# Optimization experiments

Hardware: AMD Instinct MI355X
Metric: run time of the kernel (lower is better)

The kernel has to match this reference:

```python
import jax, jax.numpy as jnp
import numpy as np

N, E, G, IN, H, L, C = 20000, 320000, 128, 16, 64, 4, 10
AVG_D_LOG = float(np.log(17.0))  # log(avg_degree + 1)


def setup_inputs() -> dict:
    key = jax.random.key(0)
    ks = jax.random.split(key, 24)
    p = lambda k, shape: jax.random.normal(k, shape, dtype=jnp.float32) * 0.05
    return dict(
        h=jax.random.normal(ks[0], (N, IN), jnp.float32),
        snorm_n=jax.random.uniform(ks[1], (N, 1), jnp.float32, 0.05, 1.0),
        embW=p(ks[2], (IN, H)), embB=p(ks[3], (H,)),
        preW=p(ks[4], (L, 2 * H, H)), preB=p(ks[5], (L, H)),
        postW=p(ks[6], (L, 13 * H, H)), postB=p(ks[7], (L, H)),
        mixW=p(ks[8], (L, H, H)), mixB=p(ks[9], (L, H)),
        r1W=p(ks[10], (H, H // 2)), r1B=p(ks[11], (H // 2,)),
        r2W=p(ks[12], (H // 2, H // 4)), r2B=p(ks[13], (H // 4,)),
        r3W=p(ks[14], (H // 4, C)), r3B=p(ks[15], (C,)),
        src=jax.random.randint(ks[16], (E,), 0, N),
        dst=jax.random.randint(ks[17], (E,), 0, N),
        graph_ids=jnp.sort(jax.random.randint(ks[18], (N,), 0, G)),
    )


def _pna_forward(h, snorm_n, embW, embB, preW, preB, postW, postB, mixW, mixB,
                 r1W, r1B, r2W, r2B, r3W, r3B, src, dst, graph_ids):
    # Degree-based scalers (computed once; graph is fixed across layers)
    deg = jax.ops.segment_sum(jnp.ones((E,), h.dtype), dst, num_segments=N)  # [N]
    degc = jnp.maximum(deg, 1.0)[:, None]
    logd = jnp.log(deg + 1.0)
    amp = (logd / AVG_D_LOG)[:, None]                      # amplification scaler
    att = (AVG_D_LOG / jnp.maximum(logd, 1e-5))[:, None]   # attenuation scaler
    has_nb = (deg > 0.0)[:, None]

    x = h @ embW + embB  # node embedding [N, H]
    for i in range(L):
        x_in = x
        # pretrans: per-edge message from cat(h_src, h_dst)  [E, H]
        m = jnp.concatenate([x[src], x[dst]], axis=-1) @ preW[i] + preB[i]
        # multi-aggregator reduce at dst: mean, max, min, std
        mean = jax.ops.segment_sum(m, dst, num_segments=N) / degc
        msq = jax.ops.segment_sum(m * m, dst, num_segments=N) / degc
        std = jnp.sqrt(jax.nn.relu(msq - mean * mean) + 1e-5)
        mx = jnp.where(has_nb, jax.ops.segment_max(m, dst, num_segments=N), 0.0)
        mn = jnp.where(has_nb, jax.ops.segment_min(m, dst, num_segments=N), 0.0)
        agg = jnp.concatenate([mean, mx, mn, std], axis=-1)  # [N, 4H]
        # degree scalers: identity, amplification, attenuation -> [N, 12H]
        scaled = jnp.concatenate([agg, agg * amp, agg * att], axis=-1)
        # posttrans over cat(scaled_agg, h) -> [N, H]
        y = jnp.concatenate([scaled, x], axis=-1) @ postW[i] + postB[i]
        # tower mixing network (LeakyReLU FC)
        y = jax.nn.leaky_relu(y @ mixW[i] + mixB[i])
        y = y * snorm_n          # graph norm
        x = x_in + y             # residual
    # mean-nodes readout per graph
    gsum = jax.ops.segment_sum(x, graph_ids, num_segments=G)
    cnt = jnp.maximum(jax.ops.segment_sum(jnp.ones((N,), x.dtype), graph_ids, num_segments=G), 1.0)
    hg = gsum / cnt[:, None]
    # MLPReadout: two halving ReLU layers + classifier
    hg = jax.nn.relu(hg @ r1W + r1B)
    hg = jax.nn.relu(hg @ r2W + r2B)
    return hg @ r3W + r3B  # [G, C]


def reference(h, snorm_n, embW, embB, preW, preB, postW, postB, mixW, mixB,
              r1W, r1B, r2W, r2B, r3W, r3B, src, dst, graph_ids):
    return _pna_forward(h, snorm_n, embW, embB, preW, preB, postW, postB,
                        mixW, mixB, r1W, r1B, r2W, r2B, r3W, r3B,
                        src, dst, graph_ids)
```

## Files before the change

kernel.cpp:

```cpp
#include <hip/hip_runtime.h>
#include <math.h>

#define N_ 20000
#define E_ 320000
#define G_ 128
#define IN_ 16
#define H_ 64
#define L_ 4
#define C_ 10
#define AVG_D_LOG 2.8332133440562162f

union F4 { float4 v; float f[4]; };

typedef _Float16 h8 __attribute__((ext_vector_type(8)));
typedef _Float16 h4 __attribute__((ext_vector_type(4)));
typedef float f4x __attribute__((ext_vector_type(4)));
#define MFMA16(a, b, c) __builtin_amdgcn_mfma_f32_16x16x32_f16((a), (b), (c), 0, 0, 0)


__global__ __launch_bounds__(256) void k_setup(
    const float* __restrict__ h, const float* __restrict__ embW, const float* __restrict__ embB,
    float* __restrict__ x,
    const float* __restrict__ preW, const float* __restrict__ postW, const float* __restrict__ mixW,
    _Float16* __restrict__ preWT, _Float16* __restrict__ postWT, _Float16* __restrict__ mixWT,
    int* __restrict__ zbase) {
  int bb = blockIdx.x, tid = threadIdx.x;
  if (bb < 5000) {
    int n = bb * 4 + (tid >> 6);
    int c = tid & 63;
    float acc = embB[c];
#pragma unroll
    for (int k = 0; k < IN_; k++) acc += h[n * IN_ + k] * embW[k * H_ + c];
    x[n * H_ + c] = acc;
  } else if (bb < 6024) {
    int idx = (bb - 5000) * 256 + tid;
    if (idx < 32768) {
      int l = idx >> 13, r = idx & 8191;
      int c = r >> 6, k = r & 63;
      preWT[idx] = (_Float16)preW[l * 8192 + k * 64 + c];
    } else if (idx < 245760) {
      int j = idx - 32768;
      int l = j / 53248, r = j % 53248;
      int c = r / 832, k = r % 832;
      postWT[j] = (_Float16)postW[l * 53248 + k * 64 + c];
    } else {
      int j = idx - 245760;
      int l = j >> 12, r = j & 4095;
      int c = r >> 6, k = r & 63;
      mixWT[j] = (_Float16)mixW[l * 4096 + k * 64 + c];
    }
  } else {
    int i = (bb - 6024) * 256 + tid;
    if (i < 2 * N_) zbase[i] = 0;
  }
}


__global__ __launch_bounds__(256) void k_hist(const int* __restrict__ dst, int* __restrict__ deg) {
  int e = blockIdx.x * 256 + threadIdx.x;
  if (e < E_) atomicAdd(&deg[dst[e]], 1);
}


__global__ __launch_bounds__(1024) void k_scan(const int* __restrict__ deg, int* __restrict__ offs) {
  __shared__ int sh[1024];
  int t = threadIdx.x;
  int base = t * 20;
  int local[20];
  int s = 0;
  if (t < 1000) {
#pragma unroll
    for (int c = 0; c < 5; c++) {
      int4 v = *(const int4*)(deg + base + c * 4);
      local[c * 4 + 0] = s; s += v.x;
      local[c * 4 + 1] = s; s += v.y;
      local[c * 4 + 2] = s; s += v.z;
      local[c * 4 + 3] = s; s += v.w;
    }
  }
  sh[t] = s;
  __syncthreads();
  for (int off = 1; off < 1024; off <<= 1) {
    int v = (t >= off) ? sh[t - off] : 0;
    __syncthreads();
    sh[t] += v;
    __syncthreads();
  }
  if (t < 1000) {
    int excl = sh[t] - s;
#pragma unroll
    for (int c = 0; c < 5; c++) {
      int4 o;
      o.x = excl + local[c * 4 + 0];
      o.y = excl + local[c * 4 + 1];
      o.z = excl + local[c * 4 + 2];
      o.w = excl + local[c * 4 + 3];
      *(int4*)(offs + base + c * 4) = o;
    }
  }
  if (t == 0) offs[N_] = sh[1023];
}


__global__ __launch_bounds__(256) void k_mix(
    const int* __restrict__ src, const int* __restrict__ dst,
    const int* __restrict__ offs, int* __restrict__ cursor, int* __restrict__ csr,
    const int* __restrict__ deg,
    float* __restrict__ ampv, float* __restrict__ attv,
    float* __restrict__ invd, float* __restrict__ hnb,
    const float* __restrict__ x, const _Float16* __restrict__ preWT,
    const float* __restrict__ preB, _Float16* __restrict__ ah, float* __restrict__ b) {
  int bb = blockIdx.x, tid = threadIdx.x;
  if (bb < 1250) {
    int e = bb * 256 + tid;
    if (e < E_) {
      int d = dst[e];
      int pos = offs[d] + atomicAdd(&cursor[d], 1);
      csr[pos] = src[e];
    }
  } else if (bb < 1329) {
    int idx = (bb - 1250) * 256 + tid;
    if (idx < N_) {
      float d = (float)deg[idx];
      float logd = logf(d + 1.f);
      ampv[idx] = logd / AVG_D_LOG;
      attv[idx] = AVG_D_LOG / fmaxf(logd, 1e-5f);
      invd[idx] = 1.f / fmaxf(d, 1.f);
      hnb[idx] = d > 0.f ? 1.f : 0.f;
    }
  } else {
    int n0 = (bb - 1329) * 32;
    int lane = tid & 63, wv = tid >> 6;
    int mt = wv & 1, nh = wv >> 1;
    int l15 = lane & 15, k0q = (lane >> 4) * 8;
    int mrow = n0 + mt * 16 + l15;
    const float* xr = x + (size_t)mrow * 64;
    const _Float16* wb0 = preWT + (size_t)(nh * 64 + l15) * 64 + k0q;
    f4x acc0 = {0.f,0.f,0.f,0.f}, acc1 = {0.f,0.f,0.f,0.f}, acc2 = {0.f,0.f,0.f,0.f}, acc3 = {0.f,0.f,0.f,0.f};
#pragma unroll
    for (int kb = 0; kb < 64; kb += 32) {
      int ko = kb + k0q;
      F4 xa, xb2;
      xa.v = *(const float4*)(xr + ko);
      xb2.v = *(const float4*)(xr + ko + 4);
      h8 af;
      af[0]=(_Float16)xa.f[0]; af[1]=(_Float16)xa.f[1]; af[2]=(_Float16)xa.f[2]; af[3]=(_Float16)xa.f[3];
      af[4]=(_Float16)xb2.f[0]; af[5]=(_Float16)xb2.f[1]; af[6]=(_Float16)xb2.f[2]; af[7]=(_Float16)xb2.f[3];
      acc0 = MFMA16(af, *(const h8*)(wb0 + kb), acc0);
      acc1 = MFMA16(af, *(const h8*)(wb0 + 1024 + kb), acc1);
      acc2 = MFMA16(af, *(const h8*)(wb0 + 2048 + kb), acc2);
      acc3 = MFMA16(af, *(const h8*)(wb0 + 3072 + kb), acc3);
    }
    int rbase = n0 + mt * 16 + (lane >> 4) * 4;
    f4x accs[4] = {acc0, acc1, acc2, acc3};
#pragma unroll
    for (int t = 0; t < 4; t++) {
      int col = nh * 64 + t * 16 + l15;
#pragma unroll
      for (int r = 0; r < 4; r++) {
        int n = rbase + r;
        if (col < 64) ah[(size_t)n * 64 + col] = (_Float16)accs[t][r];
        else          b[(size_t)n * 64 + (col - 64)] = accs[t][r] + preB[col - 64];
      }
    }
  }
}


__global__ __launch_bounds__(256, 4) void k_layer(
    const _Float16* __restrict__ ahin, const float* __restrict__ bin,
    const int* __restrict__ offs, const int* __restrict__ csr,
    const float* __restrict__ invd, const float* __restrict__ hnb,
    const _Float16* __restrict__ WT, const float* __restrict__ Bv,
    const _Float16* __restrict__ mixWT, const float* __restrict__ mixB,
    const float* __restrict__ ampv, const float* __restrict__ attv,
    const float* __restrict__ snorm, float* __restrict__ x,
    const _Float16* __restrict__ preWT, const float* __restrict__ preB,
    _Float16* __restrict__ ahout, float* __restrict__ bout, int do_pre) {
  __shared__ _Float16 aggs[16 * 280];
  __shared__ _Float16 ys[16 * 88];
  __shared__ _Float16 xs[16 * 88];
  __shared__ _Float16 xt[16 * 72];
  __shared__ int csr_s[1024];
  __shared__ int soffs[17];
  int tid = threadIdx.x;
  int n0 = blockIdx.x * 16;
  int lane = tid & 63, wv = tid >> 6;

  int e0 = offs[n0];
  int ecnt = offs[n0 + 16] - e0;
  {
    int row = tid >> 4, qq = tid & 15;
    F4 xv; xv.v = *(const float4*)(x + (size_t)(n0 + row) * 64 + qq * 4);
    h4 xh;
    xh[0] = (_Float16)xv.f[0]; xh[1] = (_Float16)xv.f[1];
    xh[2] = (_Float16)xv.f[2]; xh[3] = (_Float16)xv.f[3];
    *(h4*)(xt + row * 72 + qq * 4) = xh;
  }
  if (tid < 17) soffs[tid] = offs[n0 + tid];
  {
    int cnt = ecnt < 1024 ? ecnt : 1024;
    for (int i = tid; i < cnt; i += 256) csr_s[i] = csr[e0 + i];
  }
  __syncthreads();

  {
    int nl = tid >> 4, q = tid & 15;
    int n = n0 + nl;
    int o0 = soffs[nl];
    int deg = soffs[nl + 1] - o0;
    float inv = invd[n], hn = hnb[n];
    F4 bv; bv.v = *(const float4*)(bin + (size_t)n * 64 + q * 4);
    float sum[4], sq[4], mx[4], mn[4];
#pragma unroll
    for (int i = 0; i < 4; i++) {
      sum[i] = 0.f; sq[i] = 0.f;
      mx[i] = -__builtin_inff(); mn[i] = __builtin_inff();
    }
#define ACC4_(S0, S1, S2, S3)                                            \
    do {                                                                 \
      h4 a0 = *(const h4*)(ahin + (size_t)(S0) * 64 + q * 4);            \
      h4 a1 = *(const h4*)(ahin + (size_t)(S1) * 64 + q * 4);            \
      h4 a2 = *(const h4*)(ahin + (size_t)(S2) * 64 + q * 4);            \
      h4 a3 = *(const h4*)(ahin + (size_t)(S3) * 64 + q * 4);            \
      _Pragma("unroll")                                                  \
      for (int i = 0; i < 4; i++) {                                      \
        float v0 = (float)a0[i], v1 = (float)a1[i];                      \
        float v2 = (float)a2[i], v3 = (float)a3[i];                      \
        sum[i] += (v0 + v1) + (v2 + v3);                                 \
        sq[i] += v0 * v0; sq[i] += v1 * v1;                              \
        sq[i] += v2 * v2; sq[i] += v3 * v3;                              \
        mx[i] = fmaxf(mx[i], fmaxf(fmaxf(v0, v1), fmaxf(v2, v3)));       \
        mn[i] = fminf(mn[i], fminf(fminf(v0, v1), fminf(v2, v3)));       \
      }                                                                  \
    } while (0)
#define ACC1_(S0)                                                        \
    do {                                                                 \
      h4 a0 = *(const h4*)(ahin + (size_t)(S0) * 64 + q * 4);            \
      _Pragma("unroll")                                                  \
      for (int i = 0; i < 4; i++) {                                      \
        float v0 = (float)a0[i];                                         \
        sum[i] += v0; sq[i] += v0 * v0;                                  \
        mx[i] = fmaxf(mx[i], v0); mn[i] = fminf(mn[i], v0);              \
      }                                                                  \
    } while (0)
    if (ecnt <= 1024) {
      int lo = o0 - e0;
      int j = 0;
      for (; j + 3 < deg; j += 4) {
        int s0 = csr_s[lo + j], s1 = csr_s[lo + j + 1];
        int s2 = csr_s[lo + j + 2], s3 = csr_s[lo + j + 3];
        ACC4_(s0, s1, s2, s3);
      }
      for (; j < deg; j++) { int s0 = csr_s[lo + j]; ACC1_(s0); }
    } else {
      int j = 0;
      for (; j + 3 < deg; j += 4) {
        int s0 = csr[o0 + j], s1 = csr[o0 + j + 1];
        int s2 = csr[o0 + j + 2], s3 = csr[o0 + j + 3];
        ACC4_(s0, s1, s2, s3);
      }
      for (; j < deg; j++) { int s0 = csr[o0 + j]; ACC1_(s0); }
    }
#undef ACC4_
#undef ACC1_
    h4 hm, hx, hmn, hs;
#pragma unroll
    for (int i = 0; i < 4; i++) {
      float mean_a = sum[i] * inv;
      float var = sq[i] * inv - mean_a * mean_a;
      hs[i] = (_Float16)sqrtf(fmaxf(var, 0.f) + 1e-5f);
      bool nb = hn > 0.5f;
      hm[i] = (_Float16)(nb ? (mean_a + bv.f[i]) : 0.f);
      hx[i] = (_Float16)(nb ? (mx[i] + bv.f[i]) : 0.f);
      hmn[i] = (_Float16)(nb ? (mn[i] + bv.f[i]) : 0.f);
    }
    _Float16* ap = aggs + nl * 280 + q * 4;
    *(h4*)(ap) = hm;
    *(h4*)(ap + 64) = hx;
    *(h4*)(ap + 128) = hmn;
    *(h4*)(ap + 192) = hs;
  }
  __syncthreads();

  int nh = wv;
  int l15 = lane & 15, k0q = (lane >> 4) * 8;
  const _Float16* ag = aggs + (size_t)l15 * 280 + k0q;
  int col0 = nh * 16 + l15;
  const _Float16* w0 = WT + (size_t)col0 * 832 + k0q;
  f4x aI = {0.f,0.f,0.f,0.f}, aA = {0.f,0.f,0.f,0.f}, aT = {0.f,0.f,0.f,0.f};
#pragma unroll 4
  for (int kb = 0; kb < 256; kb += 32) {
    h8 af = *(const h8*)(ag + kb);
    aI = MFMA16(af, *(const h8*)(w0 + kb), aI);
    aA = MFMA16(af, *(const h8*)(w0 + 256 + kb), aA);
    aT = MFMA16(af, *(const h8*)(w0 + 512 + kb), aT);
  }
  const _Float16* xtr = xt + (size_t)l15 * 72 + k0q;
#pragma unroll
  for (int kb = 0; kb < 64; kb += 32) {
    h8 af = *(const h8*)(xtr + kb);
    aI = MFMA16(af, *(const h8*)(w0 + 768 + kb), aI);
  }
  int qr = (lane >> 4) * 4;
  int rbase = n0 + qr;
  int yrow = qr;
  float b0 = Bv[col0];
#pragma unroll
  for (int r = 0; r < 4; r++) {
    int n = rbase + r;
    float amp = ampv[n], att = attv[n];
    ys[(yrow + r) * 88 + col0] = (_Float16)(aI[r] + b0 + amp * aA[r] + att * aT[r]);
  }
  __syncthreads();
  f4x m0 = {0.f,0.f,0.f,0.f};
  const _Float16* yr = ys + (size_t)l15 * 88 + k0q;
  const _Float16* mw0 = mixWT + (size_t)col0 * 64 + k0q;
#pragma unroll
  for (int kb = 0; kb < 64; kb += 32) {
    h8 af = *(const h8*)(yr + kb);
    m0 = MFMA16(af, *(const h8*)(mw0 + kb), m0);
  }
  float mb0 = mixB[col0];
#pragma unroll
  for (int r = 0; r < 4; r++) {
    int n = rbase + r;
    float sn = snorm[n];
    float t0 = m0[r] + mb0; t0 = t0 > 0.f ? t0 : 0.01f * t0;
    float* xp = x + (size_t)n * 64;
    float xo0 = xp[col0] + t0 * sn;
    xp[col0] = xo0;
    xs[(yrow + r) * 88 + col0] = (_Float16)xo0;
  }

  if (do_pre) {
    __syncthreads();
    int ch = wv;
    const _Float16* xf = xs + (size_t)l15 * 88 + k0q;
    const _Float16* wb0 = preWT + (size_t)(ch * 32 + l15) * 64 + k0q;
    f4x p0 = {0.f,0.f,0.f,0.f}, p1 = {0.f,0.f,0.f,0.f};
#pragma unroll
    for (int kb = 0; kb < 64; kb += 32) {
      h8 af = *(const h8*)(xf + kb);
      p0 = MFMA16(af, *(const h8*)(wb0 + kb), p0);
      p1 = MFMA16(af, *(const h8*)(wb0 + 1024 + kb), p1);
    }
    int prb = n0 + (lane >> 4) * 4;
    f4x accs[2] = {p0, p1};
#pragma unroll
    for (int t = 0; t < 2; t++) {
      int col = ch * 32 + t * 16 + l15;
#pragma unroll
      for (int r = 0; r < 4; r++) {
        int n = prb + r;
        if (col < 64) ahout[(size_t)n * 64 + col] = (_Float16)accs[t][r];
        else          bout[(size_t)n * 64 + (col - 64)] = accs[t][r] + preB[col - 64];
      }
    }
  }
}


__device__ inline int lower_bound_gid(const int* __restrict__ gid, int val) {
  int lo = 0, hi = N_;
  while (lo < hi) {
    int mid = (lo + hi) >> 1;
    if (gid[mid] < val) lo = mid + 1; else hi = mid;
  }
  return lo;
}

__global__ __launch_bounds__(256) void k_readout_fused(
    const float* __restrict__ x, const int* __restrict__ gid,
    const float* __restrict__ r1W, const float* __restrict__ r1B,
    const float* __restrict__ r2W, const float* __restrict__ r2B,
    const float* __restrict__ r3W, const float* __restrict__ r3B,
    float* __restrict__ out) {
  __shared__ float part[4 * 64];
  __shared__ float hg[64];
  __shared__ float t1[32];
  __shared__ float t2[16];
  int g = blockIdx.x, tid = threadIdx.x;
  int lo = lower_bound_gid(gid, g);
  int hi = lower_bound_gid(gid, g + 1);
  int c = tid & 63, w = tid >> 6;
  float s = 0.f;
  for (int n = lo + w; n < hi; n += 4) s += x[(size_t)n * 64 + c];
  part[w * 64 + c] = s;
  __syncthreads();
  if (w == 0) {
    float tot = part[c] + part[64 + c] + part[128 + c] + part[192 + c];
    float cnt = (float)(hi - lo);
    if (cnt < 1.f) cnt = 1.f;
    hg[c] = tot / cnt;
  }
  __syncthreads();
  if (tid < 32) {
    float acc = r1B[tid];
#pragma unroll 8
    for (int k = 0; k < 64; k++) acc += hg[k] * r1W[k * 32 + tid];
    t1[tid] = fmaxf(acc, 0.f);
  }
  __syncthreads();
  if (tid < 16) {
    float acc = r2B[tid];
#pragma unroll 8
    for (int k = 0; k < 32; k++) acc += t1[k] * r2W[k * 16 + tid];
    t2[tid] = fmaxf(acc, 0.f);
  }
  __syncthreads();
  if (tid < 10) {
    float acc = r3B[tid];
#pragma unroll
    for (int k = 0; k < 16; k++) acc += t2[k] * r3W[k * 10 + tid];
    out[g * 10 + tid] = acc;
  }
}


extern "C" void kernel_launch(void* const* d_in, const int* in_sizes, int n_in,
                              void* d_out, int out_size, void* d_ws, size_t ws_size,
                              hipStream_t stream) {
  const float* h     = (const float*)d_in[0];
  const float* snorm = (const float*)d_in[1];
  const float* embW  = (const float*)d_in[2];
  const float* embB  = (const float*)d_in[3];
  const float* preW  = (const float*)d_in[4];
  const float* preB  = (const float*)d_in[5];
  const float* postW = (const float*)d_in[6];
  const float* postB = (const float*)d_in[7];
  const float* mixW  = (const float*)d_in[8];
  const float* mixB  = (const float*)d_in[9];
  const float* r1W   = (const float*)d_in[10];
  const float* r1B   = (const float*)d_in[11];
  const float* r2W   = (const float*)d_in[12];
  const float* r2B   = (const float*)d_in[13];
  const float* r3W   = (const float*)d_in[14];
  const float* r3B   = (const float*)d_in[15];
  const int* src     = (const int*)d_in[16];
  const int* dst     = (const int*)d_in[17];
  const int* gid     = (const int*)d_in[18];
  float* out = (float*)d_out;

  char* w = (char*)d_ws;
  float* x        = (float*)w; w += (size_t)N_ * 64 * 4;
  _Float16* ah0   = (_Float16*)w; w += (size_t)N_ * 64 * 2;
  _Float16* ah1   = (_Float16*)w; w += (size_t)N_ * 64 * 2;
  float* b0       = (float*)w; w += (size_t)N_ * 64 * 4;
  float* b1       = (float*)w; w += (size_t)N_ * 64 * 4;
  _Float16* preWT = (_Float16*)w; w += (size_t)4 * 128 * 64 * 2;
  _Float16* postWT= (_Float16*)w; w += (size_t)4 * 64 * 832 * 2;
  _Float16* mixWT = (_Float16*)w; w += (size_t)4 * 64 * 64 * 2;
  float* ampv = (float*)w; w += (size_t)N_ * 4;
  float* attv = (float*)w; w += (size_t)N_ * 4;
  float* invd = (float*)w; w += (size_t)N_ * 4;
  float* hnb  = (float*)w; w += (size_t)N_ * 4;
  int* csr    = (int*)w;   w += (size_t)E_ * 4;
  int* offs   = (int*)w;   w += (size_t)(N_ + 64) * 4;
  int* zbase  = (int*)w;
  int* deg    = (int*)w;   w += (size_t)N_ * 4;
  int* cursor = (int*)w;   w += (size_t)N_ * 4;

  k_setup<<<6181, 256, 0, stream>>>(h, embW, embB, x, preW, postW, mixW,
                                    preWT, postWT, mixWT, zbase);
  k_hist<<<E_ / 256, 256, 0, stream>>>(dst, deg);
  k_scan<<<1, 1024, 0, stream>>>(deg, offs);
  k_mix<<<1250 + 79 + 625, 256, 0, stream>>>(src, dst, offs, cursor, csr, deg,
                                             ampv, attv, invd, hnb,
                                             x, preWT, preB, ah0, b0);
  int gb = N_ / 16;
  _Float16* ahs[2] = {ah0, ah1};
  float* bs[2] = {b0, b1};
  for (int l = 0; l < L_; l++) {
    int pin = l & 1, pout = 1 - pin;
    k_layer<<<gb, 256, 0, stream>>>(ahs[pin], bs[pin], offs, csr, invd, hnb,
                                    postWT + (size_t)l * 53248, postB + l * H_,
                                    mixWT + (size_t)l * 4096, mixB + l * H_,
                                    ampv, attv, snorm, x,
                                    preWT + (size_t)(l + 1 < L_ ? l + 1 : 0) * 8192,
                                    preB + (l + 1 < L_ ? l + 1 : 0) * H_,
                                    ahs[pout], bs[pout], l + 1 < L_ ? 1 : 0);
  }
  k_readout_fused<<<G_, 256, 0, stream>>>(x, gid, r1W, r1B, r2W, r2B, r3W, r3B, out);
}
```

Before: 277.5 us.

## Tile postW transpose, prefetch gather loads, cache per-node scalars in LDS

The postW fp16 transpose in setup now goes through a shared-memory tile with coalesced float4 reads and h4 writes, replacing strided scalar accesses. k_layer software-pipelines the neighbor gather by issuing the next four loads before processing the current four. It preloads bias, scalers, snorm and the fp32 residual x into shared memory or registers early, and raises the occupancy hint to 5 blocks per SM. Readout uses 512 threads. The extra LDS and the occupancy target may increase register pressure or cause spills.

```diff
diff --git a/kernel.cpp b/kernel.cpp
--- a/kernel.cpp
+++ b/kernel.cpp
@@ -24,6 +24,7 @@
     const float* __restrict__ preW, const float* __restrict__ postW, const float* __restrict__ mixW,
     _Float16* __restrict__ preWT, _Float16* __restrict__ postWT, _Float16* __restrict__ mixWT,
     int* __restrict__ zbase) {
+  __shared__ float tl[64][68];
   int bb = blockIdx.x, tid = threadIdx.x;
   if (bb < 5000) {
     int n = bb * 4 + (tid >> 6);
@@ -32,25 +33,43 @@
 #pragma unroll
     for (int k = 0; k < IN_; k++) acc += h[n * IN_ + k] * embW[k * H_ + c];
     x[n * H_ + c] = acc;
-  } else if (bb < 6024) {
-    int idx = (bb - 5000) * 256 + tid;
+  } else if (bb < 5052) {
+    int t = bb - 5000;
+    int l = t / 13, kt = t % 13, k0 = kt * 64;
+    const float* Wsrc = postW + (size_t)l * 53248;
+    _Float16* Wdst = postWT + (size_t)l * 53248;
+    int r = tid >> 4, q4 = (tid & 15) * 4;
+#pragma unroll
+    for (int p = 0; p < 4; p++) {
+      int rr = p * 16 + r;
+      float4 v = *(const float4*)(Wsrc + (size_t)(k0 + rr) * 64 + q4);
+      tl[rr][q4 + 0] = v.x; tl[rr][q4 + 1] = v.y;
+      tl[rr][q4 + 2] = v.z; tl[rr][q4 + 3] = v.w;
+    }
+    __syncthreads();
+#pragma unroll
+    for (int p = 0; p < 4; p++) {
+      int o = p * 256 + tid;
+      int c = o >> 4, j4 = (o & 15) * 4;
+      h4 hv;
+      hv[0] = (_Float16)tl[j4 + 0][c]; hv[1] = (_Float16)tl[j4 + 1][c];
+      hv[2] = (_Float16)tl[j4 + 2][c]; hv[3] = (_Float16)tl[j4 + 3][c];
+      *(h4*)(Wdst + (size_t)c * 832 + k0 + j4) = hv;
+    }
+  } else if (bb < 5244) {
+    int idx = (bb - 5052) * 256 + tid;
     if (idx < 32768) {
       int l = idx >> 13, r = idx & 8191;
       int c = r >> 6, k = r & 63;
       preWT[idx] = (_Float16)preW[l * 8192 + k * 64 + c];
-    } else if (idx < 245760) {
+    } else {
       int j = idx - 32768;
-      int l = j / 53248, r = j % 53248;
-      int c = r / 832, k = r % 832;
-      postWT[j] = (_Float16)postW[l * 53248 + k * 64 + c];
-    } else {
-      int j = idx - 245760;
       int l = j >> 12, r = j & 4095;
       int c = r >> 6, k = r & 63;
       mixWT[j] = (_Float16)mixW[l * 4096 + k * 64 + c];
     }
   } else {
-    int i = (bb - 6024) * 256 + tid;
+    int i = (bb - 5244) * 256 + tid;
     if (i < 2 * N_) zbase[i] = 0;
   }
 }
@@ -167,7 +186,7 @@
 }
 
 
-__global__ __launch_bounds__(256, 4) void k_layer(
+__global__ __launch_bounds__(256, 5) void k_layer(
     const _Float16* __restrict__ ahin, const float* __restrict__ bin,
     const int* __restrict__ offs, const int* __restrict__ csr,
     const float* __restrict__ invd, const float* __restrict__ hnb,
@@ -180,9 +199,11 @@
   __shared__ _Float16 aggs[16 * 280];
   __shared__ _Float16 ys[16 * 88];
   __shared__ _Float16 xs[16 * 88];
-  __shared__ _Float16 xt[16 * 72];
+  __shared__ _Float16 xt[16 * 88];
+  __shared__ float xs32[16 * 68];
   __shared__ int csr_s[1024];
   __shared__ int soffs[17];
+  __shared__ float scal[48];
   int tid = threadIdx.x;
   int n0 = blockIdx.x * 16;
   int lane = tid & 63, wv = tid >> 6;
@@ -195,9 +216,22 @@
     h4 xh;
     xh[0] = (_Float16)xv.f[0]; xh[1] = (_Float16)xv.f[1];
     xh[2] = (_Float16)xv.f[2]; xh[3] = (_Float16)xv.f[3];
-    *(h4*)(xt + row * 72 + qq * 4) = xh;
+    *(h4*)(xt + row * 88 + qq * 4) = xh;
+    *(float4*)(xs32 + row * 68 + qq * 4) = xv.v;
   }
   if (tid < 17) soffs[tid] = offs[n0 + tid];
+  if (tid >= 32 && tid < 48) {
+    int i = tid - 32;
+    scal[i] = ampv[n0 + i];
+    scal[16 + i] = attv[n0 + i];
+    scal[32 + i] = snorm[n0 + i];
+  }
+  int nlA = tid >> 4, qA = tid & 15;
+  F4 bv; bv.v = *(const float4*)(bin + (size_t)(n0 + nlA) * 64 + qA * 4);
+  float inv = invd[n0 + nlA], hn = hnb[n0 + nlA];
+  int col0 = wv * 16 + (tid & 15);
+  float b0v = Bv[col0];
+  float mb0 = mixB[col0];
   {
     int cnt = ecnt < 1024 ? ecnt : 1024;
     for (int i = tid; i < cnt; i += 256) csr_s[i] = csr[e0 + i];
@@ -205,41 +239,21 @@
   __syncthreads();
 
   {
-    int nl = tid >> 4, q = tid & 15;
-    int n = n0 + nl;
+    int nl = nlA, q = qA;
     int o0 = soffs[nl];
     int deg = soffs[nl + 1] - o0;
-    float inv = invd[n], hn = hnb[n];
-    F4 bv; bv.v = *(const float4*)(bin + (size_t)n * 64 + q * 4);
     float sum[4], sq[4], mx[4], mn[4];
 #pragma unroll
     for (int i = 0; i < 4; i++) {
       sum[i] = 0.f; sq[i] = 0.f;
       mx[i] = -__builtin_inff(); mn[i] = __builtin_inff();
     }
-#define ACC4_(S0, S1, S2, S3)                                            \
+#define GLD_(S) (*(const h4*)(ahin + (size_t)(S) * 64 + q * 4))
+#define PROC1_(AV)                                                       \
     do {                                                                 \
-      h4 a0 = *(const h4*)(ahin + (size_t)(S0) * 64 + q * 4);            \
-      h4 a1 = *(const h4*)(ahin + (size_t)(S1) * 64 + q * 4);            \
-      h4 a2 = *(const h4*)(ahin + (size_t)(S2) * 64 + q * 4);            \
-      h4 a3 = *(const h4*)(ahin + (size_t)(S3) * 64 + q * 4);            \
       _Pragma("unroll")                                                  \
       for (int i = 0; i < 4; i++) {                                      \
-        float v0 = (float)a0[i], v1 = (float)a1[i];                      \
-        float v2 = (float)a2[i], v3 = (float)a3[i];                      \
-        sum[i] += (v0 + v1) + (v2 + v3);                                 \
-        sq[i] += v0 * v0; sq[i] += v1 * v1;                              \
-        sq[i] += v2 * v2; sq[i] += v3 * v3;                              \
-        mx[i] = fmaxf(mx[i], fmaxf(fmaxf(v0, v1), fmaxf(v2, v3)));       \
-        mn[i] = fminf(mn[i], fminf(fminf(v0, v1), fminf(v2, v3)));       \
-      }                                                                  \
-    } while (0)
-#define ACC1_(S0)                                                        \
-    do {                                                                 \
-      h4 a0 = *(const h4*)(ahin + (size_t)(S0) * 64 + q * 4);            \
-      _Pragma("unroll")                                                  \
-      for (int i = 0; i < 4; i++) {                                      \
-        float v0 = (float)a0[i];                                         \
+        float v0 = (float)AV[i];                                         \
         sum[i] += v0; sq[i] += v0 * v0;                                  \
         mx[i] = fmaxf(mx[i], v0); mn[i] = fminf(mn[i], v0);              \
       }                                                                  \
@@ -247,23 +261,26 @@
     if (ecnt <= 1024) {
       int lo = o0 - e0;
       int j = 0;
-      for (; j + 3 < deg; j += 4) {
-        int s0 = csr_s[lo + j], s1 = csr_s[lo + j + 1];
-        int s2 = csr_s[lo + j + 2], s3 = csr_s[lo + j + 3];
-        ACC4_(s0, s1, s2, s3);
+      h4 A0, A1, A2, A3;
+      if (j + 3 < deg) {
+        A0 = GLD_(csr_s[lo]);     A1 = GLD_(csr_s[lo + 1]);
+        A2 = GLD_(csr_s[lo + 2]); A3 = GLD_(csr_s[lo + 3]);
       }
-      for (; j < deg; j++) { int s0 = csr_s[lo + j]; ACC1_(s0); }
+      for (; j + 7 < deg; j += 4) {
+        int s0 = csr_s[lo + j + 4], s1 = csr_s[lo + j + 5];
+        int s2 = csr_s[lo + j + 6], s3 = csr_s[lo + j + 7];
+        h4 B0 = GLD_(s0), B1 = GLD_(s1), B2 = GLD_(s2), B3 = GLD_(s3);
+        PROC1_(A0); PROC1_(A1); PROC1_(A2); PROC1_(A3);
+        A0 = B0; A1 = B1; A2 = B2; A3 = B3;
+      }
+      if (j + 3 < deg) { PROC1_(A0); PROC1_(A1); PROC1_(A2); PROC1_(A3); j += 4; }
+      for (; j < deg; j++) { h4 a0 = GLD_(csr_s[lo + j]); PROC1_(a0); }
     } else {
       int j = 0;
-      for (; j + 3 < deg; j += 4) {
-        int s0 = csr[o0 + j], s1 = csr[o0 + j + 1];
-        int s2 = csr[o0 + j + 2], s3 = csr[o0 + j + 3];
-        ACC4_(s0, s1, s2, s3);
-      }
-      for (; j < deg; j++) { int s0 = csr[o0 + j]; ACC1_(s0); }
-    }
-#undef ACC4_
-#undef ACC1_
+      for (; j < deg; j++) { h4 a0 = GLD_(csr[o0 + j]); PROC1_(a0); }
+    }
+#undef GLD_
+#undef PROC1_
     h4 hm, hx, hmn, hs;
 #pragma unroll
     for (int i = 0; i < 4; i++) {
@@ -283,10 +300,8 @@
   }
   __syncthreads();
 
-  int nh = wv;
   int l15 = lane & 15, k0q = (lane >> 4) * 8;
   const _Float16* ag = aggs + (size_t)l15 * 280 + k0q;
-  int col0 = nh * 16 + l15;
   const _Float16* w0 = WT + (size_t)col0 * 832 + k0q;
   f4x aI = {0.f,0.f,0.f,0.f}, aA = {0.f,0.f,0.f,0.f}, aT = {0.f,0.f,0.f,0.f};
 #pragma unroll 4
@@ -296,7 +311,7 @@
     aA = MFMA16(af, *(const h8*)(w0 + 256 + kb), aA);
     aT = MFMA16(af, *(const h8*)(w0 + 512 + kb), aT);
   }
-  const _Float16* xtr = xt + (size_t)l15 * 72 + k0q;
+  const _Float16* xtr = xt + (size_t)l15 * 88 + k0q;
 #pragma unroll
   for (int kb = 0; kb < 64; kb += 32) {
     h8 af = *(const h8*)(xtr + kb);
@@ -304,13 +319,10 @@
   }
   int qr = (lane >> 4) * 4;
   int rbase = n0 + qr;
-  int yrow = qr;
-  float b0 = Bv[col0];
 #pragma unroll
   for (int r = 0; r < 4; r++) {
-    int n = rbase + r;
-    float amp = ampv[n], att = attv[n];
-    ys[(yrow + r) * 88 + col0] = (_Float16)(aI[r] + b0 + amp * aA[r] + att * aT[r]);
+    float amp = scal[qr + r], att = scal[16 + qr + r];
+    ys[(qr + r) * 88 + col0] = (_Float16)(aI[r] + b0v + amp * aA[r] + att * aT[r]);
   }
   __syncthreads();
   f4x m0 = {0.f,0.f,0.f,0.f};
@@ -321,16 +333,14 @@
     h8 af = *(const h8*)(yr + kb);
     m0 = MFMA16(af, *(const h8*)(mw0 + kb), m0);
   }
-  float mb0 = mixB[col0];
 #pragma unroll
   for (int r = 0; r < 4; r++) {
     int n = rbase + r;
-    float sn = snorm[n];
+    float sn = scal[32 + qr + r];
     float t0 = m0[r] + mb0; t0 = t0 > 0.f ? t0 : 0.01f * t0;
-    float* xp = x + (size_t)n * 64;
-    float xo0 = xp[col0] + t0 * sn;
-    xp[col0] = xo0;
-    xs[(yrow + r) * 88 + col0] = (_Float16)xo0;
+    float xo0 = xs32[(qr + r) * 68 + col0] + t0 * sn;
+    x[(size_t)n * 64 + col0] = xo0;
+    xs[(qr + r) * 88 + col0] = (_Float16)xo0;
   }
 
   if (do_pre) {
@@ -370,13 +380,13 @@
   return lo;
 }
 
-__global__ __launch_bounds__(256) void k_readout_fused(
+__global__ __launch_bounds__(512) void k_readout_fused(
     const float* __restrict__ x, const int* __restrict__ gid,
     const float* __restrict__ r1W, const float* __restrict__ r1B,
     const float* __restrict__ r2W, const float* __restrict__ r2B,
     const float* __restrict__ r3W, const float* __restrict__ r3B,
     float* __restrict__ out) {
-  __shared__ float part[4 * 64];
+  __shared__ float part[8 * 64];
   __shared__ float hg[64];
   __shared__ float t1[32];
   __shared__ float t2[16];
@@ -385,11 +395,13 @@
   int hi = lower_bound_gid(gid, g + 1);
   int c = tid & 63, w = tid >> 6;
   float s = 0.f;
-  for (int n = lo + w; n < hi; n += 4) s += x[(size_t)n * 64 + c];
+  for (int n = lo + w; n < hi; n += 8) s += x[(size_t)n * 64 + c];
   part[w * 64 + c] = s;
   __syncthreads();
   if (w == 0) {
-    float tot = part[c] + part[64 + c] + part[128 + c] + part[192 + c];
+    float tot = 0.f;
+#pragma unroll
+    for (int p = 0; p < 8; p++) tot += part[p * 64 + c];
     float cnt = (float)(hi - lo);
     if (cnt < 1.f) cnt = 1.f;
     hg[c] = tot / cnt;
@@ -461,7 +473,7 @@
   int* deg    = (int*)w;   w += (size_t)N_ * 4;
   int* cursor = (int*)w;   w += (size_t)N_ * 4;
 
-  k_setup<<<6181, 256, 0, stream>>>(h, embW, embB, x, preW, postW, mixW,
+  k_setup<<<5401, 256, 0, stream>>>(h, embW, embB, x, preW, postW, mixW,
                                     preWT, postWT, mixWT, zbase);
   k_hist<<<E_ / 256, 256, 0, stream>>>(dst, deg);
   k_scan<<<1, 1024, 0, stream>>>(deg, offs);
@@ -481,5 +493,5 @@
                                     preB + (l + 1 < L_ ? l + 1 : 0) * H_,
                                     ahs[pout], bs[pout], l + 1 < L_ ? 1 : 0);
   }
-  k_readout_fused<<<G_, 256, 0, stream>>>(x, gid, r1W, r1B, r2W, r2B, r3W, r3B, out);
-}
+  k_readout_fused<<<G_, 512, 0, stream>>>(x, gid, r1W, r1B, r2W, r2B, r3W, r3B, out);
+}
```

After: 273.8 us. No clear change (-1.3%).
